# Optimization experiments

Measured on AMD Instinct MI355X. Metric: run time of the kernel, lower is better.

Reference implementation:

```python
import jax, jax.numpy as jnp
import numpy as np

B, S, D = 2, 2048, 1024
N_HEAD, D_ATTN = 16, 64


def setup_inputs() -> dict:
    key = jax.random.key(0)
    ks = jax.random.split(key, 5)
    x = jax.random.normal(ks[0], (B, S, D), dtype=jnp.float32)
    # causal mask: True = masked (as consumed by torch.masked_fill)
    mask = jnp.triu(jnp.ones((S, S), dtype=bool), k=1)
    scale = 0.02
    w_q = jax.random.normal(ks[1], (D, N_HEAD * D_ATTN), dtype=jnp.float32) * scale
    w_k = jax.random.normal(ks[2], (D, N_HEAD * D_ATTN), dtype=jnp.float32) * scale
    w_v = jax.random.normal(ks[3], (D, N_HEAD * D_ATTN), dtype=jnp.float32) * scale
    w_o = jax.random.normal(ks[4], (N_HEAD * D_ATTN, D), dtype=jnp.float32) * scale
    return {"x": x, "mask": mask, "w_q": w_q, "w_k": w_k, "w_v": w_v, "w_o": w_o}


def _split(t):
    # [B,S,H*Da] -> [B,H,S,Da]
    b, s, _ = t.shape
    return t.reshape(b, s, N_HEAD, D_ATTN).transpose(0, 2, 1, 3)


def reference(x, mask, w_q, w_k, w_v, w_o):
    q = _split(x @ w_q)
    k = _split(x @ w_k)
    v = _split(x @ w_v)
    scale = D_ATTN ** 0.5
    score = jnp.einsum("bhqd,bhkd->bhqk", q, k) / scale  # [B,H,S,S]
    score = jnp.where(mask, -jnp.inf, score)
    prob = jax.nn.softmax(score, axis=-1)
    out = jnp.einsum("bhqk,bhkd->bhqd", prob, v)
    out = out.transpose(0, 2, 1, 3).reshape(x.shape[0], x.shape[1], N_HEAD * D_ATTN)
    return out @ w_o
```

## Files before the change

kernel.cpp:

```cpp
#include <hip/hip_runtime.h>
#include <stdint.h>

using u16 = unsigned short;
using u32 = unsigned int;
using u64 = unsigned long long;

typedef float f32x4 __attribute__((ext_vector_type(4)));
typedef __bf16 bf16x8 __attribute__((ext_vector_type(8)));

#define DEV static __device__ __forceinline__

DEV u16 f2bf(float f) {
  u32 u = __float_as_uint(f);
  u += 0x7FFFu + ((u >> 16) & 1u);
  return (u16)(u >> 16);
}

DEV void gld16(const void* g, void* l) {
  __builtin_amdgcn_global_load_lds((__attribute__((address_space(1))) void*)g,
                                   (__attribute__((address_space(3))) void*)l,
                                   16, 0, 0);
}

__global__ void k_cvt(const float* __restrict__ x, u16* __restrict__ xb,
                      const float* __restrict__ w0, const float* __restrict__ w1,
                      const float* __restrict__ w2, const float* __restrict__ w3,
                      u16* __restrict__ t0, u16* __restrict__ t1,
                      u16* __restrict__ t2, u16* __restrict__ t3) {
  const int tid = threadIdx.x;
  if (blockIdx.x < 2048) {
    int i = (blockIdx.x * 256 + tid) * 8;
    float4 a = *(const float4*)&x[i];
    float4 b = *(const float4*)&x[i + 4];
    __align__(16) u16 o[8];
    o[0] = f2bf(a.x); o[1] = f2bf(a.y); o[2] = f2bf(a.z); o[3] = f2bf(a.w);
    o[4] = f2bf(b.x); o[5] = f2bf(b.y); o[6] = f2bf(b.z); o[7] = f2bf(b.w);
    *(uint4*)&xb[i] = *(const uint4*)o;
    return;
  }
  const int c = blockIdx.x - 2048;
  const int z = c >> 8, rem = c & 255;
  const float* w = z == 0 ? w0 : z == 1 ? w1 : z == 2 ? w2 : w3;
  u16* wt       = z == 0 ? t0 : z == 1 ? t1 : z == 2 ? t2 : t3;
  __shared__ __align__(16) float tile[64][68];
  const int k0 = (rem & 15) * 64, n0 = (rem >> 4) * 64;
#pragma unroll
  for (int i = 0; i < 4; ++i) {
    int cc = tid + i * 256;
    int kr = cc >> 4, col = (cc & 15) * 4;
    *(float4*)&tile[kr][col] = *(const float4*)&w[(size_t)(k0 + kr) * 1024 + n0 + col];
  }
  __syncthreads();
#pragma unroll
  for (int i = 0; i < 2; ++i) {
    int cc = tid + i * 256;
    int nr = cc >> 3, kc = (cc & 7) * 8;
    __align__(16) u16 o[8];
#pragma unroll
    for (int j = 0; j < 8; ++j) o[j] = f2bf(tile[kc + j][nr]);
    *(uint4*)&wt[(size_t)(n0 + nr) * 1024 + k0 + kc] = *(const uint4*)o;
  }
}

DEV void gemm_mainloop(const u16* __restrict__ A, const u16* __restrict__ Bt,
                       int m0, int n0, u16* Asb, u16* Bsb, f32x4 (&acc)[4][4]) {
  const int tid = threadIdx.x;
  const int lane = tid & 63;
  const int wv = tid >> 6;
  const int wm = (wv >> 1) * 64, wn = (wv & 1) * 64;

#pragma unroll
  for (int i = 0; i < 4; ++i)
#pragma unroll
    for (int j = 0; j < 4; ++j) {
      f32x4 z = {0.f, 0.f, 0.f, 0.f};
      acc[i][j] = z;
    }

  const int c0 = wv * 64 + lane, c1 = c0 + 256;
  const int r0 = c0 >> 2, r1 = c1 >> 2;
  const int b0 = (c0 & 3) ^ (r0 & 3) ^ ((r0 >> 2) & 3);
  const int b1 = (c1 & 3) ^ (r1 & 3) ^ ((r1 >> 2) & 3);
  const u16* ga0 = A + (size_t)(m0 + r0) * 1024 + b0 * 8;
  const u16* ga1 = A + (size_t)(m0 + r1) * 1024 + b1 * 8;
  const u16* gb0 = Bt + (size_t)(n0 + r0) * 1024 + b0 * 8;
  const u16* gb1 = Bt + (size_t)(n0 + r1) * 1024 + b1 * 8;
  const int da0 = (wv * 64) * 8, da1 = (wv * 64 + 256) * 8;

  int aoff[4], boff[4];
#pragma unroll
  for (int f = 0; f < 4; ++f) {
    int ra = wm + f * 16 + (lane & 15);
    aoff[f] = ra * 32 + (((lane >> 4) ^ (ra & 3) ^ ((ra >> 2) & 3)) * 8);
    int rb = wn + f * 16 + (lane & 15);
    boff[f] = rb * 32 + (((lane >> 4) ^ (rb & 3) ^ ((rb >> 2) & 3)) * 8);
  }

#pragma unroll
  for (int p = 0; p < 2; ++p) {
    const int k0 = p * 32, bo = p * 4096;
    gld16(ga0 + k0, Asb + bo + da0);
    gld16(ga1 + k0, Asb + bo + da1);
    gld16(gb0 + k0, Bsb + bo + da0);
    gld16(gb1 + k0, Bsb + bo + da1);
  }

#pragma unroll 1
  for (int kt = 0; kt < 32; ++kt) {
    if (kt < 31) asm volatile("s_waitcnt vmcnt(4)" ::: "memory");
    else         asm volatile("s_waitcnt vmcnt(0)" ::: "memory");
    __builtin_amdgcn_s_barrier();
    __builtin_amdgcn_sched_barrier(0);

    if (kt + 2 < 32) {
      const int k0 = (kt + 2) * 32, bo = ((kt + 2) % 3) * 4096;
      gld16(ga0 + k0, Asb + bo + da0);
      gld16(ga1 + k0, Asb + bo + da1);
      gld16(gb0 + k0, Bsb + bo + da0);
      gld16(gb1 + k0, Bsb + bo + da1);
    }

    const int bo = (kt % 3) * 4096;
    bf16x8 af[4], bfv[4];
#pragma unroll
    for (int f = 0; f < 4; ++f) af[f] = *(const bf16x8*)&Asb[bo + aoff[f]];
#pragma unroll
    for (int f = 0; f < 4; ++f) bfv[f] = *(const bf16x8*)&Bsb[bo + boff[f]];
#pragma unroll
    for (int i = 0; i < 4; ++i)
#pragma unroll
      for (int j = 0; j < 4; ++j)
        acc[i][j] = __builtin_amdgcn_mfma_f32_16x16x32_bf16(af[i], bfv[j], acc[i][j], 0, 0, 0);
  }
}

__global__ __launch_bounds__(256) void k_gemm_qkv(
    const u16* __restrict__ X, const u16* __restrict__ Wq, const u16* __restrict__ Wk,
    const u16* __restrict__ Wv, u16* __restrict__ Q, u16* __restrict__ K,
    u16* __restrict__ V) {
  __shared__ __align__(16) u16 SH[24576];
  u16* Asb = SH;
  u16* Bsb = SH + 12288;
  const int nb = blockIdx.x, mb = blockIdx.y;
  const int proj = nb >> 3, n0 = (nb & 7) * 128;
  const u16* W = proj == 0 ? Wq : proj == 1 ? Wk : Wv;
  u16* Dst = proj == 0 ? Q : proj == 1 ? K : V;
  const float scl = proj == 0 ? 0.125f * 1.4426950408889634f : 1.0f;
  f32x4 acc[4][4];
  gemm_mainloop(X, W, mb * 128, n0, Asb, Bsb, acc);

  const int tid = threadIdx.x;
  const int lane = tid & 63, wv = tid >> 6;
  const int lo = lane & 15, hi = lane >> 4;
  const int wm = (wv >> 1) * 64, wn = (wv & 1) * 64;

  __syncthreads();
  u16 (*Ct)[132] = (u16(*)[132])SH;
#pragma unroll
  for (int i = 0; i < 4; ++i)
#pragma unroll
    for (int j = 0; j < 4; ++j)
#pragma unroll
      for (int r = 0; r < 4; ++r)
        Ct[wm + i * 16 + hi * 4 + r][wn + j * 16 + lo] = f2bf(acc[i][j][r] * scl);
  __syncthreads();

  const int b = (mb * 128) >> 11;
  const int sbase = (mb * 128) & 2047;
  const int h0 = n0 >> 6;
#pragma unroll
  for (int p = 0; p < 8; ++p) {
    const int row = p * 16 + (tid >> 4);
    const int ch = tid & 15;
    const int h = h0 + (ch >> 3), d = (ch & 7) * 8;
    __align__(16) u16 o[8];
#pragma unroll
    for (int q = 0; q < 8; ++q) o[q] = Ct[row][ch * 8 + q];
    *(uint4*)&Dst[(size_t)((b * 16 + h) * 2048 + sbase + row) * 64 + d] = *(const uint4*)o;
  }
}

__global__ __launch_bounds__(256) void k_gemm_out(
    const u16* __restrict__ A, const u16* __restrict__ Wt, float* __restrict__ Out) {
  __shared__ __align__(16) u16 Asb[3 * 4096];
  __shared__ __align__(16) u16 Bsb[3 * 4096];
  const int nb = blockIdx.x, mb = blockIdx.y;
  f32x4 acc[4][4];
  gemm_mainloop(A, Wt, mb * 128, nb * 128, Asb, Bsb, acc);
  const int lane = threadIdx.x & 63, wv = threadIdx.x >> 6;
  const int wm = (wv >> 1) * 64, wn = (wv & 1) * 64;
#pragma unroll
  for (int i = 0; i < 4; ++i)
#pragma unroll
    for (int j = 0; j < 4; ++j)
#pragma unroll
      for (int r = 0; r < 4; ++r) {
        int m = mb * 128 + wm + i * 16 + (lane >> 4) * 4 + r;
        int n = nb * 128 + wn + j * 16 + (lane & 15);
        Out[(size_t)m * 1024 + n] = acc[i][j][r];
      }
}

__global__ void k_transpose_v(const u16* __restrict__ V, u16* __restrict__ Vt) {
  __shared__ __align__(16) u16 t[64][80];
  const int bh = blockIdx.y, s0 = blockIdx.x * 64;
  const int tid = threadIdx.x;
#pragma unroll
  for (int i = 0; i < 2; ++i) {
    int c = tid + i * 256;
    int sr = c >> 3, dc = (c & 7) * 8;
    *(uint4*)&t[sr][dc] = *(const uint4*)&V[((size_t)bh * 2048 + s0 + sr) * 64 + dc];
  }
  __syncthreads();
#pragma unroll
  for (int i = 0; i < 2; ++i) {
    int c = tid + i * 256;
    int dr = c >> 3, c7 = c & 7;
    __align__(8) u16 o[8];
#pragma unroll
    for (int j = 0; j < 8; ++j) o[j] = t[c7 * 8 + j][dr];
    int bp = ((c7 >> 1) & 1) * 32 + (c7 & 1) * 16 + ((c7 >> 2) & 1) * 4;
    u16* row = &Vt[((size_t)bh * 64 + dr) * 2048 + s0];
    *(u64*)&row[bp]     = *(const u64*)&o[0];
    *(u64*)&row[bp + 8] = *(const u64*)&o[4];
  }
}

DEV void qk_tile(const u16* Kc, const bf16x8 (&qf)[2], int lo, int hi, f32x4 (&sc)[4]) {
#pragma unroll
  for (int cf = 0; cf < 4; ++cf) {
    f32x4 z = {0.f, 0.f, 0.f, 0.f};
    sc[cf] = z;
#pragma unroll
    for (int kf = 0; kf < 2; ++kf) {
      int row = cf * 16 + lo;
      int blk = ((kf * 4 + hi) ^ (row & 7)) * 8;
      bf16x8 kfr = *(const bf16x8*)&Kc[row * 64 + blk];
      sc[cf] = __builtin_amdgcn_mfma_f32_16x16x32_bf16(kfr, qf[kf], sc[cf], 0, 0, 0);
    }
  }
}

DEV void sm_pv(f32x4 (&sc)[4], const u16* Vc, int lane, int lo, int hi,
               float& m_run, float& l_run, f32x4 (&ao)[4]) {
  float mx0 = fmaxf(fmaxf(sc[0][0], sc[0][1]), fmaxf(sc[0][2], sc[0][3]));
  float mx1 = fmaxf(fmaxf(sc[1][0], sc[1][1]), fmaxf(sc[1][2], sc[1][3]));
  float mx2 = fmaxf(fmaxf(sc[2][0], sc[2][1]), fmaxf(sc[2][2], sc[2][3]));
  float mx3 = fmaxf(fmaxf(sc[3][0], sc[3][1]), fmaxf(sc[3][2], sc[3][3]));
  float mx = fmaxf(fmaxf(mx0, mx1), fmaxf(mx2, mx3));
  mx = fmaxf(mx, __shfl_xor(mx, 16));
  mx = fmaxf(mx, __shfl_xor(mx, 32));

  if (__any(mx > m_run + 8.0f)) {
    float mnew = fmaxf(m_run, mx);
    float sclf = __builtin_amdgcn_exp2f(m_run - mnew);
    const int base = lane & 48;
#pragma unroll
    for (int r = 0; r < 4; ++r) {
      float s_r = __shfl(sclf, base + hi * 4 + r);
#pragma unroll
      for (int df = 0; df < 4; ++df) ao[df][r] *= s_r;
    }
    l_run *= sclf;
    m_run = mnew;
  }

  float pp[4];
  bf16x8 pa0, pa1;
#pragma unroll
  for (int cf = 0; cf < 4; ++cf) {
    float p0 = __builtin_amdgcn_exp2f(sc[cf][0] - m_run);
    float p1 = __builtin_amdgcn_exp2f(sc[cf][1] - m_run);
    float p2 = __builtin_amdgcn_exp2f(sc[cf][2] - m_run);
    float p3 = __builtin_amdgcn_exp2f(sc[cf][3] - m_run);
    pp[cf] = (p0 + p1) + (p2 + p3);
    bf16x8& pa = (cf & 1) ? pa1 : pa0;
    int j = (cf >> 1) * 4;
    pa[j] = (__bf16)p0; pa[j + 1] = (__bf16)p1;
    pa[j + 2] = (__bf16)p2; pa[j + 3] = (__bf16)p3;
  }
  float psum = (pp[0] + pp[1]) + (pp[2] + pp[3]);
  psum += __shfl_xor(psum, 16);
  psum += __shfl_xor(psum, 32);
  l_run += psum;

  __builtin_amdgcn_s_setprio(1);
#pragma unroll
  for (int df = 0; df < 4; ++df) {
#pragma unroll
    for (int kf = 0; kf < 2; ++kf) {
      int row = df * 16 + lo;
      int blk = ((kf * 4 + hi) ^ (row & 7)) * 8;
      bf16x8 vfr = *(const bf16x8*)&Vc[row * 64 + blk];
      ao[df] = __builtin_amdgcn_mfma_f32_16x16x32_bf16(kf == 0 ? pa0 : pa1, vfr,
                                                       ao[df], 0, 0, 0);
    }
  }
  __builtin_amdgcn_s_setprio(0);
}

__global__ __launch_bounds__(512) void k_attn(
    const u16* __restrict__ Qg, const u16* __restrict__ Kg,
    const u16* __restrict__ Vtg, u16* __restrict__ Og) {
  __shared__ __align__(16) u16 Ks[4][64 * 64];
  __shared__ __align__(16) u16 Vs[4][64 * 64];
  const int tid = threadIdx.x, lane = tid & 63, wv = tid >> 6;
  const int lo = lane & 15, hi = lane >> 4;
  const int w4 = wv & 3, qsel = wv >> 2;

  const int flat = blockIdx.y * 16 + blockIdx.x;
  const int xcd = flat & 7, slot = flat >> 3;
  const int bh = xcd * 4 + (slot >> 4);
  const int jp = slot & 15;

  const u16* Qb = Qg + (size_t)bh * 2048 * 64;
  const u16* Kb = Kg + (size_t)bh * 2048 * 64;
  const u16* Vb = Vtg + (size_t)bh * 64 * 2048;
  const int b = bh >> 4, h = bh & 15;

  const int nta = jp + 1, ntb = 32 - jp;
  const int q0 = (qsel ? (31 - jp) : jp) * 64;
  const int myNt = qsel ? ntb : nta;
  const int qq = q0 + w4 * 16 + lo;

  bf16x8 qf[2];
#pragma unroll
  for (int kf = 0; kf < 2; ++kf)
    qf[kf] = *(const bf16x8*)&Qb[(size_t)(q0 + w4 * 16 + lo) * 64 + kf * 32 + hi * 8];

  f32x4 ao[4];
#pragma unroll
  for (int df = 0; df < 4; ++df) {
    f32x4 z = {0.f, 0.f, 0.f, 0.f};
    ao[df] = z;
  }
  float m_run = -1e30f, l_run = 0.f;

  const int r0 = tid >> 3;
  const int e0 = ((tid & 7) ^ (r0 & 7)) * 8;

#pragma unroll
  for (int p = 0; p < 3; ++p) {
    gld16(Kb + (size_t)(p * 64 + r0) * 64 + e0, &Ks[p][wv * 512]);
    gld16(Vb + (size_t)r0 * 2048 + p * 64 + e0, &Vs[p][wv * 512]);
  }

#pragma unroll 1
  for (int t = 0; t < ntb; ++t) {
    if (t + 2 < ntb)      asm volatile("s_waitcnt vmcnt(4)" ::: "memory");
    else if (t + 1 < ntb) asm volatile("s_waitcnt vmcnt(2)" ::: "memory");
    else                  asm volatile("s_waitcnt vmcnt(0)" ::: "memory");
    __builtin_amdgcn_s_barrier();
    __builtin_amdgcn_sched_barrier(0);

    if (t + 3 < ntb) {
      const int kn = (t + 3) * 64;
      gld16(Kb + (size_t)(kn + r0) * 64 + e0, &Ks[(t + 3) & 3][wv * 512]);
      gld16(Vb + (size_t)r0 * 2048 + kn + e0, &Vs[(t + 3) & 3][wv * 512]);
    }

    if (t < myNt) {
      const u16* Kc = Ks[t & 3];
      const u16* Vc = Vs[t & 3];
      f32x4 sc[4];
      __builtin_amdgcn_s_setprio(1);
      qk_tile(Kc, qf, lo, hi, sc);
      __builtin_amdgcn_s_setprio(0);

      if (t == myNt - 1) {
        const int kv0 = t * 64;
#pragma unroll
        for (int cf = 0; cf < 4; ++cf)
#pragma unroll
          for (int r = 0; r < 4; ++r) {
            int kk = kv0 + cf * 16 + hi * 4 + r;
            if (kk > qq) sc[cf][r] = -1e30f;
          }
      }

      sm_pv(sc, Vc, lane, lo, hi, m_run, l_run, ao);
    }
  }

  float linv[4];
  const int base = lane & 48;
#pragma unroll
  for (int r = 0; r < 4; ++r) {
    float l_r = __shfl(l_run, base + hi * 4 + r);
    linv[r] = 1.0f / l_r;
  }
#pragma unroll
  for (int df = 0; df < 4; ++df)
#pragma unroll
    for (int r = 0; r < 4; ++r) {
      int s = q0 + w4 * 16 + hi * 4 + r;
      int d = df * 16 + lo;
      Og[((size_t)(b * 2048 + s)) * 1024 + h * 64 + d] = f2bf(ao[df][r] * linv[r]);
    }
}

extern "C" void kernel_launch(void* const* d_in, const int* in_sizes, int n_in,
                              void* d_out, int out_size, void* d_ws, size_t ws_size,
                              hipStream_t stream) {
  const float* x = (const float*)d_in[0];
  const float* wq = (const float*)d_in[2];
  const float* wk = (const float*)d_in[3];
  const float* wv = (const float*)d_in[4];
  const float* wo = (const float*)d_in[5];

  char* ws = (char*)d_ws;
  u16* xb  = (u16*)(ws);
  u16* wqt = (u16*)(ws + 8388608);
  u16* wkt = (u16*)(ws + 8388608 + 2097152);
  u16* wvt = (u16*)(ws + 8388608 + 2 * 2097152);
  u16* wot = (u16*)(ws + 8388608 + 3 * 2097152);
  u16* qb  = (u16*)(ws + 16777216);
  u16* kb  = (u16*)(ws + 16777216 + 8388608);
  u16* vb  = (u16*)(ws + 16777216 + 2 * 8388608);
  u16* vt  = (u16*)(ws + 16777216 + 3 * 8388608);
  u16* ao  = (u16*)(ws + 16777216 + 4 * 8388608);

  k_cvt<<<dim3(3072), dim3(256), 0, stream>>>(x, xb, wq, wk, wv, wo, wqt, wkt, wvt, wot);
  k_gemm_qkv<<<dim3(24, 32), dim3(256), 0, stream>>>(xb, wqt, wkt, wvt, qb, kb, vb);
  k_transpose_v<<<dim3(32, 32), dim3(256), 0, stream>>>(vb, vt);
  k_attn<<<dim3(16, 32), dim3(512), 0, stream>>>(qb, kb, vt, ao);
  k_gemm_out<<<dim3(8, 32), dim3(256), 0, stream>>>(ao, wot, (float*)d_out);
}
```

Before: 119.0 us.

## Fuse V transpose into QKV GEMM epilogue and reorder attention block scheduling

The V projection tiles are now transposed through shared memory inside the QKV GEMM epilogue and written straight into the permuted Vt layout, which removes the separate transpose kernel launch and its extra round trip of V through global memory. The attention kernel also maps workgroups to query-pair indices in reversed order for alternate bh groups, to even out causal work across each XCD. The new epilogue writes 8-byte chunks with a strided pattern, which may coalesce less well than the previous 16-byte row stores.

```diff
diff --git a/kernel.cpp b/kernel.cpp
--- a/kernel.cpp
+++ b/kernel.cpp
@@ -137,14 +137,13 @@
 __global__ __launch_bounds__(256) void k_gemm_qkv(
     const u16* __restrict__ X, const u16* __restrict__ Wq, const u16* __restrict__ Wk,
     const u16* __restrict__ Wv, u16* __restrict__ Q, u16* __restrict__ K,
-    u16* __restrict__ V) {
+    u16* __restrict__ Vt) {
   __shared__ __align__(16) u16 SH[24576];
   u16* Asb = SH;
   u16* Bsb = SH + 12288;
   const int nb = blockIdx.x, mb = blockIdx.y;
   const int proj = nb >> 3, n0 = (nb & 7) * 128;
   const u16* W = proj == 0 ? Wq : proj == 1 ? Wk : Wv;
-  u16* Dst = proj == 0 ? Q : proj == 1 ? K : V;
   const float scl = proj == 0 ? 0.125f * 1.4426950408889634f : 1.0f;
   f32x4 acc[4][4];
   gemm_mainloop(X, W, mb * 128, n0, Asb, Bsb, acc);
@@ -153,30 +152,54 @@
   const int lane = tid & 63, wv = tid >> 6;
   const int lo = lane & 15, hi = lane >> 4;
   const int wm = (wv >> 1) * 64, wn = (wv & 1) * 64;
-
-  __syncthreads();
-  u16 (*Ct)[132] = (u16(*)[132])SH;
-#pragma unroll
-  for (int i = 0; i < 4; ++i)
-#pragma unroll
-    for (int j = 0; j < 4; ++j)
-#pragma unroll
-      for (int r = 0; r < 4; ++r)
-        Ct[wm + i * 16 + hi * 4 + r][wn + j * 16 + lo] = f2bf(acc[i][j][r] * scl);
-  __syncthreads();
-
   const int b = (mb * 128) >> 11;
   const int sbase = (mb * 128) & 2047;
   const int h0 = n0 >> 6;
-#pragma unroll
-  for (int p = 0; p < 8; ++p) {
-    const int row = p * 16 + (tid >> 4);
-    const int ch = tid & 15;
-    const int h = h0 + (ch >> 3), d = (ch & 7) * 8;
-    __align__(16) u16 o[8];
-#pragma unroll
-    for (int q = 0; q < 8; ++q) o[q] = Ct[row][ch * 8 + q];
-    *(uint4*)&Dst[(size_t)((b * 16 + h) * 2048 + sbase + row) * 64 + d] = *(const uint4*)o;
+
+  __syncthreads();
+
+  if (proj == 2) {
+    u16 (*Ctv)[132] = (u16(*)[132])SH;
+#pragma unroll
+    for (int i = 0; i < 4; ++i)
+#pragma unroll
+      for (int j = 0; j < 4; ++j)
+#pragma unroll
+        for (int r = 0; r < 4; ++r)
+          Ctv[wn + j * 16 + lo][wm + i * 16 + hi * 4 + r] = f2bf(acc[i][j][r]);
+    __syncthreads();
+    const int g = tid & 15;
+    const int bp = ((g >> 2) & 1) * 32 + ((g >> 1) & 1) * 16 + (g & 1) * 8 +
+                   ((g >> 3) & 1) * 4;
+#pragma unroll
+    for (int p = 0; p < 16; ++p) {
+      const int ci = p * 16 + (tid >> 4);
+      const int blk = ci & 1, d = (ci >> 1) & 63, hl = ci >> 7;
+      u64 v = *(const u64*)&Ctv[hl * 64 + d][blk * 64 + g * 4];
+      *(u64*)&Vt[((size_t)((b * 16 + h0 + hl) * 64 + d)) * 2048 +
+                 sbase + blk * 64 + bp] = v;
+    }
+  } else {
+    u16* Dst = proj == 0 ? Q : K;
+    u16 (*Ct)[132] = (u16(*)[132])SH;
+#pragma unroll
+    for (int i = 0; i < 4; ++i)
+#pragma unroll
+      for (int j = 0; j < 4; ++j)
+#pragma unroll
+        for (int r = 0; r < 4; ++r)
+          Ct[wm + i * 16 + hi * 4 + r][wn + j * 16 + lo] = f2bf(acc[i][j][r] * scl);
+    __syncthreads();
+#pragma unroll
+    for (int p = 0; p < 8; ++p) {
+      const int row = p * 16 + (tid >> 4);
+      const int ch = tid & 15;
+      const int h = h0 + (ch >> 3), d = (ch & 7) * 8;
+      __align__(16) u16 o[8];
+#pragma unroll
+      for (int q = 0; q < 8; ++q) o[q] = Ct[row][ch * 8 + q];
+      *(uint4*)&Dst[(size_t)((b * 16 + h) * 2048 + sbase + row) * 64 + d] = *(const uint4*)o;
+    }
   }
 }
 
@@ -199,31 +222,6 @@
         int n = nb * 128 + wn + j * 16 + (lane & 15);
         Out[(size_t)m * 1024 + n] = acc[i][j][r];
       }
-}
-
-__global__ void k_transpose_v(const u16* __restrict__ V, u16* __restrict__ Vt) {
-  __shared__ __align__(16) u16 t[64][80];
-  const int bh = blockIdx.y, s0 = blockIdx.x * 64;
-  const int tid = threadIdx.x;
-#pragma unroll
-  for (int i = 0; i < 2; ++i) {
-    int c = tid + i * 256;
-    int sr = c >> 3, dc = (c & 7) * 8;
-    *(uint4*)&t[sr][dc] = *(const uint4*)&V[((size_t)bh * 2048 + s0 + sr) * 64 + dc];
-  }
-  __syncthreads();
-#pragma unroll
-  for (int i = 0; i < 2; ++i) {
-    int c = tid + i * 256;
-    int dr = c >> 3, c7 = c & 7;
-    __align__(8) u16 o[8];
-#pragma unroll
-    for (int j = 0; j < 8; ++j) o[j] = t[c7 * 8 + j][dr];
-    int bp = ((c7 >> 1) & 1) * 32 + (c7 & 1) * 16 + ((c7 >> 2) & 1) * 4;
-    u16* row = &Vt[((size_t)bh * 64 + dr) * 2048 + s0];
-    *(u64*)&row[bp]     = *(const u64*)&o[0];
-    *(u64*)&row[bp + 8] = *(const u64*)&o[4];
-  }
 }
 
 DEV void qk_tile(const u16* Kc, const bf16x8 (&qf)[2], int lo, int hi, f32x4 (&sc)[4]) {
@@ -310,8 +308,9 @@
 
   const int flat = blockIdx.y * 16 + blockIdx.x;
   const int xcd = flat & 7, slot = flat >> 3;
-  const int bh = xcd * 4 + (slot >> 4);
-  const int jp = slot & 15;
+  const int q4 = slot >> 4, rsl = slot & 15;
+  const int bh = xcd * 4 + q4;
+  const int jp = (q4 & 2) ? (15 - rsl) : rsl;
 
   const u16* Qb = Qg + (size_t)bh * 2048 * 64;
   const u16* Kb = Kg + (size_t)bh * 2048 * 64;
@@ -416,13 +415,11 @@
   u16* wot = (u16*)(ws + 8388608 + 3 * 2097152);
   u16* qb  = (u16*)(ws + 16777216);
   u16* kb  = (u16*)(ws + 16777216 + 8388608);
-  u16* vb  = (u16*)(ws + 16777216 + 2 * 8388608);
   u16* vt  = (u16*)(ws + 16777216 + 3 * 8388608);
   u16* ao  = (u16*)(ws + 16777216 + 4 * 8388608);
 
   k_cvt<<<dim3(3072), dim3(256), 0, stream>>>(x, xb, wq, wk, wv, wo, wqt, wkt, wvt, wot);
-  k_gemm_qkv<<<dim3(24, 32), dim3(256), 0, stream>>>(xb, wqt, wkt, wvt, qb, kb, vb);
-  k_transpose_v<<<dim3(32, 32), dim3(256), 0, stream>>>(vb, vt);
+  k_gemm_qkv<<<dim3(24, 32), dim3(256), 0, stream>>>(xb, wqt, wkt, wvt, qb, kb, vt);
   k_attn<<<dim3(16, 32), dim3(512), 0, stream>>>(qb, kb, vt, ao);
   k_gemm_out<<<dim3(8, 32), dim3(256), 0, stream>>>(ao, wot, (float*)d_out);
 }
```

Measured after the change: 115.3 us. 1.03x faster.
